# Optimization experiments

Hardware: AMD Instinct MI355X
Metric: run time of the kernel (lower is better)

## Reference

```python
import jax, jax.numpy as jnp
import numpy as np

N, E = 100000, 1200000
IN_DIM, HID, OUT = 128, 64, 64
EPS = 1e-5


def _glorot(key, shape):
    lim = 1.0 / np.sqrt(shape[0])
    return jax.random.uniform(key, shape, jnp.float32, -lim, lim)


def setup_inputs() -> dict:
    key = jax.random.key(0)
    ks = jax.random.split(key, 20)
    inp = {
        'x': jax.random.normal(ks[0], (N, IN_DIM), jnp.float32),
        'edge_index': jax.random.randint(ks[1], (2, E), 0, N, jnp.int64),
        'xgb_scores': jax.random.uniform(ks[2], (N,), jnp.float32),
        # SAGEConv params: W_l (aggregated path, with bias), W_r (root path, no bias)
        'W1l': _glorot(ks[3], (IN_DIM, HID)), 'b1': jnp.zeros((HID,), jnp.float32), 'W1r': _glorot(ks[4], (IN_DIM, HID)),
        'g1': jnp.ones((HID,), jnp.float32), 'be1': jnp.zeros((HID,), jnp.float32),
        'W2l': _glorot(ks[5], (HID, HID)), 'b2': jnp.zeros((HID,), jnp.float32), 'W2r': _glorot(ks[6], (HID, HID)),
        'g2': jnp.ones((HID,), jnp.float32), 'be2': jnp.zeros((HID,), jnp.float32),
        'W3l': _glorot(ks[7], (HID, OUT)), 'b3': jnp.zeros((OUT,), jnp.float32), 'W3r': _glorot(ks[8], (HID, OUT)),
        'g3': jnp.ones((OUT,), jnp.float32), 'be3': jnp.zeros((OUT,), jnp.float32),
        # fusion MLP: Linear(out+1, 64) -> ReLU -> Linear(64, 1)
        'Wf1': _glorot(ks[9], (OUT + 1, 64)), 'bf1': jnp.zeros((64,), jnp.float32),
        'Wf2': _glorot(ks[10], (64, 1)), 'bf2': jnp.zeros((1,), jnp.float32),
    }
    return inp


def _sage_conv(x, src, dst, Wl, b, Wr, n):
    # mean aggregation of source features at destination nodes (PyG SAGEConv, aggr='mean')
    agg = jax.ops.segment_sum(x[src], dst, num_segments=n)           # (N, d)
    cnt = jax.ops.segment_sum(jnp.ones((src.shape[0],), x.dtype), dst, num_segments=n)
    mean = agg / jnp.clip(cnt, 1.0)[:, None]
    return mean @ Wl + b + x @ Wr


def _bn(h, g, b):
    mu = jnp.mean(h, axis=0)
    var = jnp.var(h, axis=0)  # biased, as in torch BN training normalization
    return (h - mu) * jax.lax.rsqrt(var + EPS) * g + b


def reference(x, edge_index, xgb_scores,
              W1l, b1, W1r, g1, be1,
              W2l, b2, W2r, g2, be2,
              W3l, b3, W3r, g3, be3,
              Wf1, bf1, Wf2, bf2):
    n = x.shape[0]
    src, dst = edge_index[0], edge_index[1]
    # dropout is identity in eval; BN uses batch statistics
    h = jax.nn.relu(_bn(_sage_conv(x, src, dst, W1l, b1, W1r, n), g1, be1))
    h = jax.nn.relu(_bn(_sage_conv(h, src, dst, W2l, b2, W2r, n), g2, be2))
    h = jax.nn.relu(_bn(_sage_conv(h, src, dst, W3l, b3, W3r, n), g3, be3))
    combined = jnp.concatenate([h, xgb_scores[:, None]], axis=1)     # (N, out+1)
    z = jax.nn.relu(combined @ Wf1 + bf1)
    logits = (z @ Wf2 + bf2)[:, 0]
    return logits
```

## Files before the change

### kernel.cpp

```cpp
#include <hip/hip_runtime.h>


typedef __attribute__((ext_vector_type(8))) short bf16x8;
typedef __attribute__((ext_vector_type(4))) float f32x4;

#define ELLS 48

__device__ __forceinline__ ushort f2bf(float f) {
  unsigned u = __float_as_uint(f);
  return (ushort)((u + 0x7fff + ((u >> 16) & 1)) >> 16);
}
__device__ __forceinline__ float bf2f(ushort h) {
  return __uint_as_float((unsigned)h << 16);
}
__device__ __forceinline__ void unpack8(uint4 v, float* f) {
  f[0] = __uint_as_float(v.x << 16);
  f[1] = __uint_as_float(v.x & 0xffff0000u);
  f[2] = __uint_as_float(v.y << 16);
  f[3] = __uint_as_float(v.y & 0xffff0000u);
  f[4] = __uint_as_float(v.z << 16);
  f[5] = __uint_as_float(v.z & 0xffff0000u);
  f[6] = __uint_as_float(v.w << 16);
  f[7] = __uint_as_float(v.w & 0xffff0000u);
}


__device__ __forceinline__ void prep_one(const float* __restrict__ Wl,
                                         const float* __restrict__ Wr,
                                         ushort* __restrict__ Whi,
                                         ushort* __restrict__ Wlo, int din,
                                         int i) {
  int col = i / din, k = i % din;
  float v = (col < 64) ? Wl[(size_t)k * 64 + col]
                       : Wr[(size_t)k * 64 + (col - 64)];
  ushort h = f2bf(v);
  Whi[i] = h;
  Wlo[i] = f2bf(v - bf2f(h));
}

__global__ __launch_bounds__(256) void prep_all(
    const float* __restrict__ W1l, const float* __restrict__ W1r,
    ushort* __restrict__ Whi1, ushort* __restrict__ Wlo1,
    const float* __restrict__ W2l, const float* __restrict__ W2r,
    ushort* __restrict__ Whi2, ushort* __restrict__ Wlo2,
    const float* __restrict__ W3l, const float* __restrict__ W3r,
    ushort* __restrict__ Whi3, ushort* __restrict__ Wlo3,
    int* __restrict__ deg, float* __restrict__ stats,
    ushort* __restrict__ sent, int n, int nbd) {
  int bid = blockIdx.x;
  const int tid = threadIdx.x;
  if (bid < nbd) {
    int i = bid * 256 + tid;
    if (i < n + 4) deg[i] = 0;
    return;
  }
  bid -= nbd;
  if (bid < 64) {
    prep_one(W1l, W1r, Whi1, Wlo1, 128, bid * 256 + tid);
    return;
  }
  bid -= 64;
  if (bid < 32) {
    prep_one(W2l, W2r, Whi2, Wlo2, 64, bid * 256 + tid);
    return;
  }
  bid -= 32;
  if (bid < 32) {
    prep_one(W3l, W3r, Whi3, Wlo3, 64, bid * 256 + tid);
    return;
  }
  if (tid < 384) stats[tid] = 0.f;
  if (tid < 64) sent[tid] = 0;
}


__global__ __launch_bounds__(256) void fill_gemm1(
    const int* __restrict__ ei, int* __restrict__ deg, int* __restrict__ ell,
    int E, int n, int bps, const float* __restrict__ X,
    const float* __restrict__ bias, const ushort* __restrict__ Whi,
    const ushort* __restrict__ Wlo, ushort* __restrict__ Ybf,
    ushort* __restrict__ Yrbf, int F, int G) {
  constexpr int WS = 40;
  __shared__ ushort sW[2 * 128 * WS];
  __shared__ float sB[64];
  const int tid = threadIdx.x;
  const int bid = blockIdx.x;
  const int tot = F + G;
  const int gin = (int)(((long long)(bid + 1) * G) / tot);
  const int gex = (int)(((long long)bid * G) / tot);

  if (gin == gex) {
    const int fid = bid - gex;
    const int shard = fid / bps;
    const int bib = fid & (bps - 1);
    const int chunk = n >> 3;
    const int lo = shard * chunk;
    const int hi = (shard == 7) ? n : lo + chunk;
    for (int e = bib * 256 + tid; e < E; e += bps * 256) {
      int d = __builtin_nontemporal_load(ei + E + e);
      if (d >= lo && d < hi) {
        int s = __builtin_nontemporal_load(ei + e);
        int pos = atomicAdd(&deg[d], 1);
        if (pos < ELLS) ell[(size_t)d * ELLS + pos] = s;
      }
    }
    return;
  }

  const int tile = gex;
  const int w = tid >> 6;
  const int lane = tid & 63;
  const int m = lane & 15;
  const int quad = lane >> 4;
  const int row0 = tile * 64;

  if (tid < 64) sB[tid] = bias[tid];

  const int arow = min(row0 + w * 16 + m, n - 1);

  f32x4 acc[8];
#pragma unroll
  for (int t = 0; t < 8; t++) acc[t] = (f32x4){0.f, 0.f, 0.f, 0.f};

  for (int kc = 0; kc < 128; kc += 32) {
    __syncthreads();
    for (int i = tid; i < 512; i += 256) {
      int col = i >> 2;
      int k = (i & 3) * 8;
      *reinterpret_cast<uint4*>(sW + col * WS + k) =
          *reinterpret_cast<const uint4*>(Whi + (size_t)col * 128 + kc + k);
      *reinterpret_cast<uint4*>(sW + 128 * WS + col * WS + k) =
          *reinterpret_cast<const uint4*>(Wlo + (size_t)col * 128 + kc + k);
    }
    __syncthreads();

    const int kb = kc + quad * 8;
    float av[8];
    const float* ap = X + (size_t)arow * 128 + kb;
    float4 a0 = *reinterpret_cast<const float4*>(ap);
    float4 a1 = *reinterpret_cast<const float4*>(ap + 4);
    av[0] = a0.x; av[1] = a0.y; av[2] = a0.z; av[3] = a0.w;
    av[4] = a1.x; av[5] = a1.y; av[6] = a1.z; av[7] = a1.w;
    bf16x8 Ahi, Alo;
#pragma unroll
    for (int j = 0; j < 8; j++) {
      ushort h = f2bf(av[j]);
      Ahi[j] = (short)h;
      Alo[j] = (short)f2bf(av[j] - bf2f(h));
    }
#pragma unroll
    for (int t = 0; t < 8; t++) {
      bf16x8 Bhi =
          *reinterpret_cast<const bf16x8*>(sW + (t * 16 + m) * WS + quad * 8);
      bf16x8 Blo = *reinterpret_cast<const bf16x8*>(sW + 128 * WS +
                                                    (t * 16 + m) * WS +
                                                    quad * 8);
      acc[t] = __builtin_amdgcn_mfma_f32_16x16x32_bf16(Ahi, Bhi, acc[t], 0, 0, 0);
      acc[t] = __builtin_amdgcn_mfma_f32_16x16x32_bf16(Ahi, Blo, acc[t], 0, 0, 0);
      acc[t] = __builtin_amdgcn_mfma_f32_16x16x32_bf16(Alo, Bhi, acc[t], 0, 0, 0);
    }
  }

#pragma unroll
  for (int t = 0; t < 8; t++) {
    int col = t * 16 + m;
#pragma unroll
    for (int r = 0; r < 4; r++) {
      int grow = row0 + w * 16 + quad * 4 + r;
      if (grow < n) {
        float v = acc[t][r];
        if (t < 4) {
          Ybf[(size_t)grow * 64 + col] = f2bf(v);
        } else {
          Yrbf[(size_t)grow * 64 + (col - 64)] = f2bf(v + sB[col - 64]);
        }
      }
    }
  }
}

template <int DIN, bool NORM, bool XBF16>
__global__ __launch_bounds__(256) void gemm_mfma(
    const void* __restrict__ Xv, const float* __restrict__ stats,
    const float* __restrict__ g, const float* __restrict__ be,
    const float* __restrict__ bias, const ushort* __restrict__ Whi,
    const ushort* __restrict__ Wlo, ushort* __restrict__ Ybf,
    ushort* __restrict__ Yrbf, int n) {
  constexpr int WS = 40;
  __shared__ ushort sW[2 * 128 * WS];
  __shared__ float sSS[128];
  __shared__ float sB[64];
  const int tid = threadIdx.x;
  const int w = tid >> 6;
  const int lane = tid & 63;
  const int m = lane & 15;
  const int quad = lane >> 4;
  const int row0 = blockIdx.x * 64;

  if (tid < 64) {
    sB[tid] = bias[tid];
    if (NORM) {
      float invn = 1.0f / (float)n;
      float mu = stats[tid] * invn;
      float var = fmaf(-mu, mu, stats[64 + tid] * invn);
      float sc = g[tid] * rsqrtf(var + 1e-5f);
      sSS[tid] = sc;
      sSS[64 + tid] = fmaf(-mu, sc, be[tid]);
    }
  }

  const int arow = min(row0 + w * 16 + m, n - 1);

  f32x4 acc[8];
#pragma unroll
  for (int t = 0; t < 8; t++) acc[t] = (f32x4){0.f, 0.f, 0.f, 0.f};

  for (int kc = 0; kc < DIN; kc += 32) {
    __syncthreads();
    for (int i = tid; i < 512; i += 256) {
      int col = i >> 2;
      int k = (i & 3) * 8;
      *reinterpret_cast<uint4*>(sW + col * WS + k) =
          *reinterpret_cast<const uint4*>(Whi + (size_t)col * DIN + kc + k);
      *reinterpret_cast<uint4*>(sW + 128 * WS + col * WS + k) =
          *reinterpret_cast<const uint4*>(Wlo + (size_t)col * DIN + kc + k);
    }
    __syncthreads();

    const int kb = kc + quad * 8;
    float av[8];
    if (XBF16) {
      const ushort* X = (const ushort*)Xv;
      uint4 v = *reinterpret_cast<const uint4*>(X + (size_t)arow * DIN + kb);
      unpack8(v, av);
    } else {
      const float* X = (const float*)Xv;
      const float* ap = X + (size_t)arow * DIN + kb;
      float4 a0 = *reinterpret_cast<const float4*>(ap);
      float4 a1 = *reinterpret_cast<const float4*>(ap + 4);
      av[0] = a0.x; av[1] = a0.y; av[2] = a0.z; av[3] = a0.w;
      av[4] = a1.x; av[5] = a1.y; av[6] = a1.z; av[7] = a1.w;
    }
    if (NORM) {
#pragma unroll
      for (int j = 0; j < 8; j++)
        av[j] = fmaxf(fmaf(av[j], sSS[kb + j], sSS[64 + kb + j]), 0.f);
    }
    bf16x8 Ahi, Alo;
#pragma unroll
    for (int j = 0; j < 8; j++) {
      ushort h = f2bf(av[j]);
      Ahi[j] = (short)h;
      Alo[j] = (short)f2bf(av[j] - bf2f(h));
    }
#pragma unroll
    for (int t = 0; t < 8; t++) {
      bf16x8 Bhi =
          *reinterpret_cast<const bf16x8*>(sW + (t * 16 + m) * WS + quad * 8);
      bf16x8 Blo = *reinterpret_cast<const bf16x8*>(sW + 128 * WS +
                                                    (t * 16 + m) * WS +
                                                    quad * 8);
      acc[t] = __builtin_amdgcn_mfma_f32_16x16x32_bf16(Ahi, Bhi, acc[t], 0, 0, 0);
      acc[t] = __builtin_amdgcn_mfma_f32_16x16x32_bf16(Ahi, Blo, acc[t], 0, 0, 0);
      acc[t] = __builtin_amdgcn_mfma_f32_16x16x32_bf16(Alo, Bhi, acc[t], 0, 0, 0);
    }
  }

#pragma unroll
  for (int t = 0; t < 8; t++) {
    int col = t * 16 + m;
#pragma unroll
    for (int r = 0; r < 4; r++) {
      int grow = row0 + w * 16 + quad * 4 + r;
      if (grow < n) {
        float v = acc[t][r];
        if (t < 4) {
          Ybf[(size_t)grow * 64 + col] = f2bf(v);
        } else {
          Yrbf[(size_t)grow * 64 + (col - 64)] = f2bf(v + sB[col - 64]);
        }
      }
    }
  }
}

__global__ __launch_bounds__(256) void gather_combine(
    const ushort* __restrict__ Ybf, const ushort* __restrict__ Yrbf,
    const int* __restrict__ ell, const int* __restrict__ deg,
    ushort* __restrict__ Tbf, float* __restrict__ stats, int n) {
  const int lane = threadIdx.x & 63;
  const int w = threadIdx.x >> 6;
  const int grp = lane >> 3;
  const int sub = lane & 7;
  const int wid = blockIdx.x * 4 + w;
  const int nw = gridDim.x * 4;
  float ssum[8], ssq[8];
#pragma unroll
  for (int c = 0; c < 8; c++) ssum[c] = ssq[c] = 0.f;

  for (int base = wid * 4; base < n; base += nw * 4) {
    int4 dg4 = *reinterpret_cast<const int4*>(deg + base);
    int dg[4] = {dg4.x, dg4.y, dg4.z, dg4.w};
    int mx = 0;
#pragma unroll
    for (int j = 0; j < 4; j++) mx = max(mx, min(dg[j], ELLS));
    float a[4][8];
#pragma unroll
    for (int j = 0; j < 4; j++)
#pragma unroll
      for (int c = 0; c < 8; c++) a[j][c] = 0.f;

    for (int e0 = 0; e0 < mx; e0 += 8) {
      int idx = e0 + grp;
      int s0 = ell[(size_t)(base + 0) * ELLS + idx];
      int s1 = ell[(size_t)(base + 1) * ELLS + idx];
      int s2 = ell[(size_t)(base + 2) * ELLS + idx];
      int s3 = ell[(size_t)(base + 3) * ELLS + idx];
      s0 = (idx < dg[0]) ? s0 : n;
      s1 = (idx < dg[1]) ? s1 : n;
      s2 = (idx < dg[2]) ? s2 : n;
      s3 = (idx < dg[3]) ? s3 : n;
      uint4 v0 = *reinterpret_cast<const uint4*>(Ybf + (size_t)s0 * 64 + sub * 8);
      uint4 v1 = *reinterpret_cast<const uint4*>(Ybf + (size_t)s1 * 64 + sub * 8);
      uint4 v2 = *reinterpret_cast<const uint4*>(Ybf + (size_t)s2 * 64 + sub * 8);
      uint4 v3 = *reinterpret_cast<const uint4*>(Ybf + (size_t)s3 * 64 + sub * 8);
      float f[8];
      unpack8(v0, f);
#pragma unroll
      for (int c = 0; c < 8; c++) a[0][c] += f[c];
      unpack8(v1, f);
#pragma unroll
      for (int c = 0; c < 8; c++) a[1][c] += f[c];
      unpack8(v2, f);
#pragma unroll
      for (int c = 0; c < 8; c++) a[2][c] += f[c];
      unpack8(v3, f);
#pragma unroll
      for (int c = 0; c < 8; c++) a[3][c] += f[c];
    }
#pragma unroll
    for (int mmask = 8; mmask <= 32; mmask <<= 1)
#pragma unroll
      for (int j = 0; j < 4; j++)
#pragma unroll
        for (int c = 0; c < 8; c++)
          a[j][c] += __shfl_xor(a[j][c], mmask, 64);

    if (lane < 8) {
#pragma unroll
      for (int j = 0; j < 4; j++) {
        int node = base + j;
        if (node >= n) continue;
        float iv = 1.0f / (float)max(dg[j], 1);
        uint4 yrv =
            *reinterpret_cast<const uint4*>(Yrbf + (size_t)node * 64 + sub * 8);
        float yr[8];
        unpack8(yrv, yr);
        float t[8];
#pragma unroll
        for (int c = 0; c < 8; c++) {
          t[c] = fmaf(a[j][c], iv, yr[c]);
          ssum[c] += t[c];
          ssq[c] = fmaf(t[c], t[c], ssq[c]);
        }
        uint4 o;
        o.x = (uint)f2bf(t[0]) | ((uint)f2bf(t[1]) << 16);
        o.y = (uint)f2bf(t[2]) | ((uint)f2bf(t[3]) << 16);
        o.z = (uint)f2bf(t[4]) | ((uint)f2bf(t[5]) << 16);
        o.w = (uint)f2bf(t[6]) | ((uint)f2bf(t[7]) << 16);
        *reinterpret_cast<uint4*>(Tbf + (size_t)node * 64 + sub * 8) = o;
      }
    }
  }
  __shared__ float rS[4][64];
  __shared__ float rQ[4][64];
  if (lane < 8) {
#pragma unroll
    for (int c = 0; c < 8; c++) {
      rS[w][sub * 8 + c] = ssum[c];
      rQ[w][sub * 8 + c] = ssq[c];
    }
  }
  __syncthreads();
  if (threadIdx.x < 64) {
    int tc = threadIdx.x;
    float s = rS[0][tc] + rS[1][tc] + rS[2][tc] + rS[3][tc];
    float qq = rQ[0][tc] + rQ[1][tc] + rQ[2][tc] + rQ[3][tc];
    atomicAdd(&stats[tc], s);
    atomicAdd(&stats[64 + tc], qq);
  }
}


__global__ __launch_bounds__(256) void fusion_fused(
    const ushort* __restrict__ Tbf, const float* __restrict__ stats,
    const float* __restrict__ g, const float* __restrict__ be,
    const float* __restrict__ xgb, const float* __restrict__ Wf1,
    const float* __restrict__ bf1, const float* __restrict__ Wf2,
    const float* __restrict__ bf2, float* __restrict__ out, int n) {
  __shared__ float sH[64 * 64];
  __shared__ float sW1[65 * 64];
  __shared__ float sW2[64];
  __shared__ float sSS[128];
  const int tid = threadIdx.x;
  const int c = tid & 63;
  const int w = tid >> 6;
  const int row0 = blockIdx.x * 64;
  if (tid < 64) {
    float invn = 1.0f / (float)n;
    float mu = stats[tid] * invn;
    float var = fmaf(-mu, mu, stats[64 + tid] * invn);
    float sc = g[tid] * rsqrtf(var + 1e-5f);
    sSS[tid] = sc;
    sSS[64 + tid] = fmaf(-mu, sc, be[tid]);
  }
  for (int i = tid; i < 65 * 64; i += 256) sW1[i] = Wf1[i];
  if (tid < 64) sW2[tid] = Wf2[tid];
  __syncthreads();
  for (int i = tid; i < 512; i += 256) {
    int r = i >> 3;
    int k = (i & 7) * 8;
    int row = min(row0 + r, n - 1);
    uint4 v = *reinterpret_cast<const uint4*>(Tbf + (size_t)row * 64 + k);
    float f[8];
    unpack8(v, f);
#pragma unroll
    for (int j = 0; j < 8; j++)
      f[j] = fmaxf(fmaf(f[j], sSS[k + j], sSS[64 + k + j]), 0.f);
    *reinterpret_cast<float4*>(sH + r * 64 + k) =
        make_float4(f[0], f[1], f[2], f[3]);
    *reinterpret_cast<float4*>(sH + r * 64 + k + 4) =
        make_float4(f[4], f[5], f[6], f[7]);
  }
  __syncthreads();
  const float b1v = bf1[c];
  const float wx = sW1[64 * 64 + c];
  const float w2v = sW2[c];
  const float b2v = bf2[0];
  float acc[16];
#pragma unroll
  for (int r = 0; r < 16; r++) acc[r] = b1v;
  for (int kk = 0; kk < 64; kk += 4) {
    float4 hv[16];
#pragma unroll
    for (int r = 0; r < 16; r++)
      hv[r] = *reinterpret_cast<const float4*>(sH + (w * 16 + r) * 64 + kk);
    float w0 = sW1[(kk + 0) * 64 + c];
    float w1 = sW1[(kk + 1) * 64 + c];
    float w2 = sW1[(kk + 2) * 64 + c];
    float w3 = sW1[(kk + 3) * 64 + c];
#pragma unroll
    for (int r = 0; r < 16; r++) {
      acc[r] = fmaf(hv[r].x, w0, acc[r]);
      acc[r] = fmaf(hv[r].y, w1, acc[r]);
      acc[r] = fmaf(hv[r].z, w2, acc[r]);
      acc[r] = fmaf(hv[r].w, w3, acc[r]);
    }
  }
#pragma unroll
  for (int r = 0; r < 16; r++) {
    int row = row0 + w * 16 + r;
    float xv = (row < n) ? xgb[row] : 0.f;
    float z = fmaxf(fmaf(xv, wx, acc[r]), 0.f) * w2v;
#pragma unroll
    for (int off = 32; off > 0; off >>= 1) z += __shfl_xor(z, off, 64);
    if (row < n && c == 0) out[row] = z + b2v;
  }
}


extern "C" void kernel_launch(void* const* d_in, const int* in_sizes, int n_in,
                              void* d_out, int out_size, void* d_ws,
                              size_t ws_size, hipStream_t stream) {
  const float* x = (const float*)d_in[0];
  const int* ei = (const int*)d_in[1];
  const float* xgb = (const float*)d_in[2];
  const float* W1l = (const float*)d_in[3];
  const float* b1 = (const float*)d_in[4];
  const float* W1r = (const float*)d_in[5];
  const float* g1 = (const float*)d_in[6];
  const float* be1 = (const float*)d_in[7];
  const float* W2l = (const float*)d_in[8];
  const float* b2 = (const float*)d_in[9];
  const float* W2r = (const float*)d_in[10];
  const float* g2 = (const float*)d_in[11];
  const float* be2 = (const float*)d_in[12];
  const float* W3l = (const float*)d_in[13];
  const float* b3 = (const float*)d_in[14];
  const float* W3r = (const float*)d_in[15];
  const float* g3 = (const float*)d_in[16];
  const float* be3 = (const float*)d_in[17];
  const float* Wf1 = (const float*)d_in[18];
  const float* bf1 = (const float*)d_in[19];
  const float* Wf2 = (const float*)d_in[20];
  const float* bf2 = (const float*)d_in[21];
  float* out = (float*)d_out;

  const int n = in_sizes[2];
  const int E = in_sizes[1] / 2;

  char* w = (char*)d_ws;
  auto alloc = [&](size_t bytes) {
    void* p = (void*)w;
    w += (bytes + 255) & ~(size_t)255;
    return p;
  };
  int* deg = (int*)alloc((size_t)(n + 4) * 4);
  int* ell = (int*)alloc((size_t)(n + 4) * ELLS * 4);
  ushort* Ybf = (ushort*)alloc((size_t)(n + 1) * 64 * 2);
  ushort* Yrbf = (ushort*)alloc((size_t)n * 64 * 2);
  ushort* Tbf = (ushort*)alloc((size_t)n * 64 * 2);
  ushort* Whi1 = (ushort*)alloc(128 * 128 * 2);
  ushort* Wlo1 = (ushort*)alloc(128 * 128 * 2);
  ushort* Whi2 = (ushort*)alloc(128 * 64 * 2);
  ushort* Wlo2 = (ushort*)alloc(128 * 64 * 2);
  ushort* Whi3 = (ushort*)alloc(128 * 64 * 2);
  ushort* Wlo3 = (ushort*)alloc(128 * 64 * 2);
  float* stats = (float*)alloc(3 * 128 * 4);

  const int nbd = (n + 4 + 255) / 256;
  prep_all<<<nbd + 64 + 32 + 32 + 1, 256, 0, stream>>>(
      W1l, W1r, Whi1, Wlo1, W2l, W2r, Whi2, Wlo2, W3l, W3r, Whi3, Wlo3, deg,
      stats, Ybf + (size_t)n * 64, n, nbd);

  const int gTile = (n + 63) / 64;
  const int gGath = 2048;

  const int bps = 2048;
  const int F = 8 * bps;
  const int G = gTile;
  fill_gemm1<<<F + G, 256, 0, stream>>>(ei, deg, ell, E, n, bps, x, b1, Whi1,
                                        Wlo1, Ybf, Yrbf, F, G);
  gather_combine<<<gGath, 256, 0, stream>>>(Ybf, Yrbf, ell, deg, Tbf,
                                            stats + 0, n);

  gemm_mfma<64, true, true><<<gTile, 256, 0, stream>>>(
      Tbf, stats + 0, g1, be1, b2, Whi2, Wlo2, Ybf, Yrbf, n);
  gather_combine<<<gGath, 256, 0, stream>>>(Ybf, Yrbf, ell, deg, Tbf,
                                            stats + 128, n);

  gemm_mfma<64, true, true><<<gTile, 256, 0, stream>>>(
      Tbf, stats + 128, g2, be2, b3, Whi3, Wlo3, Ybf, Yrbf, n);
  gather_combine<<<gGath, 256, 0, stream>>>(Ybf, Yrbf, ell, deg, Tbf,
                                            stats + 256, n);

  fusion_fused<<<gTile, 256, 0, stream>>>(Tbf, stats + 256, g3, be3, xgb, Wf1,
                                          bf1, Wf2, bf2, out, n);
}
```

Baseline: 483.3 us.

## Replace sharded ELL fill with single-pass vectorized edge scatter before GEMM blocks

The ELL adjacency fill no longer uses 8 destination-range shards that each rescan the whole dst array. Each fill thread now reads 8 edges with int4 loads and does the atomic degree increments and ELL writes in one pass. Fill blocks are placed first in the grid instead of being interleaved with the GEMM tiles. This cuts edge-index reads roughly eightfold, but atomics and scattered writes are no longer confined to a node range per shard, so they lose locality.

```diff
diff --git a/kernel.cpp b/kernel.cpp
--- a/kernel.cpp
+++ b/kernel.cpp
@@ -76,30 +76,45 @@
 
 __global__ __launch_bounds__(256) void fill_gemm1(
     const int* __restrict__ ei, int* __restrict__ deg, int* __restrict__ ell,
-    int E, int n, int bps, const float* __restrict__ X,
-    const float* __restrict__ bias, const ushort* __restrict__ Whi,
-    const ushort* __restrict__ Wlo, ushort* __restrict__ Ybf,
-    ushort* __restrict__ Yrbf, int F, int G) {
+    int E, int n, const float* __restrict__ X, const float* __restrict__ bias,
+    const ushort* __restrict__ Whi, const ushort* __restrict__ Wlo,
+    ushort* __restrict__ Ybf, ushort* __restrict__ Yrbf, int F, int G) {
   constexpr int WS = 40;
   __shared__ ushort sW[2 * 128 * WS];
   __shared__ float sB[64];
   const int tid = threadIdx.x;
   const int bid = blockIdx.x;
-  const int tot = F + G;
-  const int gin = (int)(((long long)(bid + 1) * G) / tot);
-  const int gex = (int)(((long long)bid * G) / tot);
-
-  if (gin == gex) {
-    const int fid = bid - gex;
-    const int shard = fid / bps;
-    const int bib = fid & (bps - 1);
-    const int chunk = n >> 3;
-    const int lo = shard * chunk;
-    const int hi = (shard == 7) ? n : lo + chunk;
-    for (int e = bib * 256 + tid; e < E; e += bps * 256) {
-      int d = __builtin_nontemporal_load(ei + E + e);
-      if (d >= lo && d < hi) {
-        int s = __builtin_nontemporal_load(ei + e);
+
+  if (bid < F) {
+    const long long base = ((long long)bid * 256 + tid) * 8;
+    if ((E & 7) == 0) {
+      if (base < E) {
+        const int b = (int)base;
+        int4 da = *reinterpret_cast<const int4*>(ei + E + b);
+        int4 db = *reinterpret_cast<const int4*>(ei + E + b + 4);
+        int4 sa = *reinterpret_cast<const int4*>(ei + b);
+        int4 sb = *reinterpret_cast<const int4*>(ei + b + 4);
+        int p0 = atomicAdd(&deg[da.x], 1);
+        int p1 = atomicAdd(&deg[da.y], 1);
+        int p2 = atomicAdd(&deg[da.z], 1);
+        int p3 = atomicAdd(&deg[da.w], 1);
+        int p4 = atomicAdd(&deg[db.x], 1);
+        int p5 = atomicAdd(&deg[db.y], 1);
+        int p6 = atomicAdd(&deg[db.z], 1);
+        int p7 = atomicAdd(&deg[db.w], 1);
+        if (p0 < ELLS) ell[(size_t)da.x * ELLS + p0] = sa.x;
+        if (p1 < ELLS) ell[(size_t)da.y * ELLS + p1] = sa.y;
+        if (p2 < ELLS) ell[(size_t)da.z * ELLS + p2] = sa.z;
+        if (p3 < ELLS) ell[(size_t)da.w * ELLS + p3] = sa.w;
+        if (p4 < ELLS) ell[(size_t)db.x * ELLS + p4] = sb.x;
+        if (p5 < ELLS) ell[(size_t)db.y * ELLS + p5] = sb.y;
+        if (p6 < ELLS) ell[(size_t)db.z * ELLS + p6] = sb.z;
+        if (p7 < ELLS) ell[(size_t)db.w * ELLS + p7] = sb.w;
+      }
+    } else {
+      for (long long e = base; e < base + 8 && e < E; ++e) {
+        int d = ei[E + e];
+        int s = ei[e];
         int pos = atomicAdd(&deg[d], 1);
         if (pos < ELLS) ell[(size_t)d * ELLS + pos] = s;
       }
@@ -107,7 +122,7 @@
     return;
   }
 
-  const int tile = gex;
+  const int tile = bid - F;
   const int w = tid >> 6;
   const int lane = tid & 63;
   const int m = lane & 15;
@@ -526,11 +541,10 @@
   const int gTile = (n + 63) / 64;
   const int gGath = 2048;
 
-  const int bps = 2048;
-  const int F = 8 * bps;
+  const int F = (E + 8 * 256 - 1) / (8 * 256);
   const int G = gTile;
-  fill_gemm1<<<F + G, 256, 0, stream>>>(ei, deg, ell, E, n, bps, x, b1, Whi1,
-                                        Wlo1, Ybf, Yrbf, F, G);
+  fill_gemm1<<<F + G, 256, 0, stream>>>(ei, deg, ell, E, n, x, b1, Whi1, Wlo1,
+                                        Ybf, Yrbf, F, G);
   gather_combine<<<gGath, 256, 0, stream>>>(Ybf, Yrbf, ell, deg, Tbf,
                                             stats + 0, n);
 
```

After: 509.6 us. 5.4% more time.

## Vectorize ELL fill edge loads and reorder fill/GEMM block scheduling

Applied to the files above, without the earlier changes.

The ELL-fill path now reads destination and source indices as int4 vectors, four edges per thread, and always loads the sources instead of only on a shard match. Fill blocks shard-interleave (shard = bid&7) and all come before the GEMM tiles rather than being interleaved with them proportionally, and blocks per shard drop from 2048 to 128. The aim is fewer load instructions and less launch overhead for the edge-list scan, which each of the 8 shards re-reads. The cost is reading the source indices unconditionally and scheduling the GEMM tiles only after all fill blocks have been dispatched.

```diff
diff --git a/kernel.cpp b/kernel.cpp
--- a/kernel.cpp
+++ b/kernel.cpp
@@ -85,21 +85,39 @@
   __shared__ float sB[64];
   const int tid = threadIdx.x;
   const int bid = blockIdx.x;
-  const int tot = F + G;
-  const int gin = (int)(((long long)(bid + 1) * G) / tot);
-  const int gex = (int)(((long long)bid * G) / tot);
-
-  if (gin == gex) {
-    const int fid = bid - gex;
-    const int shard = fid / bps;
-    const int bib = fid & (bps - 1);
+
+  if (bid < F) {
+    const int shard = bid & 7;
+    const int bib = bid >> 3;
     const int chunk = n >> 3;
     const int lo = shard * chunk;
     const int hi = (shard == 7) ? n : lo + chunk;
-    for (int e = bib * 256 + tid; e < E; e += bps * 256) {
-      int d = __builtin_nontemporal_load(ei + E + e);
-      if (d >= lo && d < hi) {
-        int s = __builtin_nontemporal_load(ei + e);
+    const int stride = bps * 256 * 4;
+    const int E4 = E & ~3;
+    for (int e = (bib * 256 + tid) * 4; e < E4; e += stride) {
+      int4 d4 = *reinterpret_cast<const int4*>(ei + E + e);
+      int4 s4 = *reinterpret_cast<const int4*>(ei + e);
+      if (d4.x >= lo && d4.x < hi) {
+        int p = atomicAdd(&deg[d4.x], 1);
+        if (p < ELLS) ell[(size_t)d4.x * ELLS + p] = s4.x;
+      }
+      if (d4.y >= lo && d4.y < hi) {
+        int p = atomicAdd(&deg[d4.y], 1);
+        if (p < ELLS) ell[(size_t)d4.y * ELLS + p] = s4.y;
+      }
+      if (d4.z >= lo && d4.z < hi) {
+        int p = atomicAdd(&deg[d4.z], 1);
+        if (p < ELLS) ell[(size_t)d4.z * ELLS + p] = s4.z;
+      }
+      if (d4.w >= lo && d4.w < hi) {
+        int p = atomicAdd(&deg[d4.w], 1);
+        if (p < ELLS) ell[(size_t)d4.w * ELLS + p] = s4.w;
+      }
+    }
+    if (shard == 0 && bib == 0) {
+      for (int e = E4 + tid; e < E; e += 256) {
+        int d = ei[E + e];
+        int s = ei[e];
         int pos = atomicAdd(&deg[d], 1);
         if (pos < ELLS) ell[(size_t)d * ELLS + pos] = s;
       }
@@ -107,7 +125,7 @@
     return;
   }
 
-  const int tile = gex;
+  const int tile = bid - F;
   const int w = tid >> 6;
   const int lane = tid & 63;
   const int m = lane & 15;
@@ -526,7 +544,7 @@
   const int gTile = (n + 63) / 64;
   const int gGath = 2048;
 
-  const int bps = 2048;
+  const int bps = 128;
   const int F = 8 * bps;
   const int G = gTile;
   fill_gemm1<<<F + G, 256, 0, stream>>>(ei, deg, ell, E, n, bps, x, b1, Whi1,
```

Result: faster. 463.7 us (-4.1%).
